# Performance work log

Hardware: AMD Instinct MI355X
Metric: run time of the kernel (lower is better)

Reference implementation:

```python
import jax, jax.numpy as jnp
import numpy as np

DIM = 96
D_STATE = 16
EXPAND = 2
D_INNER = EXPAND * DIM


def _scan_1d(x, delta, A, Bm, Cm, D):
    # x, delta: [b, l, d]; A: [d, n]; Bm, Cm: [b, l, n]; D: [d]
    delta = jax.nn.softplus(delta)
    dA = jnp.exp(jnp.einsum('bld,dn->bldn', delta, A))          # [b,l,d,n]
    dBx = jnp.einsum('bld,bln,bld->bldn', delta, Bm, x)         # delta*B*x

    def step(h, inp):
        dA_t, dBx_t, C_t = inp
        h = dA_t * h + dBx_t                                     # [b,d,n]
        y = jnp.einsum('bdn,bn->bd', h, C_t)
        return h, y

    b, l, d = x.shape
    n = A.shape[1]
    h0 = jnp.zeros((b, d, n), dtype=x.dtype)
    xs = (jnp.moveaxis(dA, 1, 0), jnp.moveaxis(dBx, 1, 0), jnp.moveaxis(Cm, 1, 0))
    _, ys = jax.lax.scan(step, h0, xs)                           # ys: [l,b,d]
    y = jnp.moveaxis(ys, 0, 1)                                   # [b,l,d]
    return y + x * D


def setup_inputs() -> dict:
    key = jax.random.key(0)
    ks = jax.random.split(key, 6)
    x = jax.random.normal(ks[0], (4, 64, 64, DIM), dtype=jnp.float32)
    d_out = D_INNER * 2 + D_STATE * 2 + D_INNER
    W_in = jax.random.normal(ks[1], (d_out, DIM), dtype=jnp.float32) * 0.02
    w_conv = jax.random.normal(ks[2], (D_INNER, 1, 3), dtype=jnp.float32) * 0.1
    W_fuse = jax.random.normal(ks[3], (D_INNER, D_INNER * 2, 1), dtype=jnp.float32) * 0.02
    W_out = jax.random.normal(ks[4], (DIM, D_INNER), dtype=jnp.float32) * 0.02
    A_log = jnp.log(jnp.tile(jnp.arange(1, D_STATE + 1, dtype=jnp.float32), (D_INNER, 1)))
    D = jnp.ones((D_INNER,), dtype=jnp.float32)
    return {"x": x, "W_in": W_in, "w_conv": w_conv, "W_fuse": W_fuse,
            "W_out": W_out, "A_log": A_log, "D": D}


def reference(x, W_in, w_conv, W_fuse, W_out, A_log, D):
    B, H, W, C = x.shape
    di, n = A_log.shape
    proj = x @ W_in.T
    x_inner, z, B_ssm, C_ssm, delta = jnp.split(
        proj, [di, 2 * di, 2 * di + n, 2 * di + 2 * n], axis=-1)
    # depthwise conv1d over length-1 sequences (kernel=3, pad=1): only center tap
    x_conv = jax.nn.silu(x_inner * w_conv[:, 0, 1])
    A = -jnp.exp(A_log)
    # horizontal scan: rows of length W
    y_h = _scan_1d(x_conv.reshape(B * H, W, di), delta.reshape(B * H, W, di), A,
                   B_ssm.reshape(B * H, W, n), C_ssm.reshape(B * H, W, n), D)
    y_h = y_h.reshape(B, H, W, di)
    # vertical scan: columns of length H
    xv = jnp.transpose(x_conv, (0, 2, 1, 3)).reshape(B * W, H, di)
    dv = jnp.transpose(delta, (0, 2, 1, 3)).reshape(B * W, H, di)
    Bv = jnp.transpose(B_ssm, (0, 2, 1, 3)).reshape(B * W, H, n)
    Cv = jnp.transpose(C_ssm, (0, 2, 1, 3)).reshape(B * W, H, n)
    y_v = _scan_1d(xv, dv, A, Bv, Cv, D).reshape(B, W, H, di)
    y_v = jnp.transpose(y_v, (0, 2, 1, 3))
    y_cat = jnp.concatenate([y_h, y_v], axis=-1)                 # [B,H,W,2*di]
    # 1x1 conv on length-1 sequences == linear map
    y_fused = jnp.einsum('bhwk,dk->bhwd', y_cat, W_fuse[:, :, 0])
    y_fused = y_fused * jax.nn.silu(z)
    return y_fused @ W_out.T
```

## Files before the change

kernel.cpp:

```cpp
#include <hip/hip_runtime.h>
#include <math.h>

#define NT    16384
#define CIN   96
#define DI    192
#define NS    16
#define SEQ   64
#define NSEQ  256

typedef __attribute__((ext_vector_type(8))) short bf16x8;
typedef __attribute__((ext_vector_type(4))) float f32x4;

__device__ __forceinline__ float silu_f(float v) {
    return v * (1.0f / (1.0f + __expf(-v)));
}

__device__ __forceinline__ float softplus_f(float v) {
    return fmaxf(v, 0.0f) + log1pf(__expf(-fabsf(v)));
}

__device__ __forceinline__ unsigned short bf16_rn(float f) {
    unsigned int u = __float_as_uint(f);
    u += 0x7FFFu + ((u >> 16) & 1u);
    return (unsigned short)(u >> 16);
}
__device__ __forceinline__ float bf16f(unsigned short h) {
    return __uint_as_float(((unsigned int)h) << 16);
}

__device__ __forceinline__ void split8(const float* __restrict__ src,
                                       bf16x8* dH, bf16x8* dL) {
    const float4 v0 = *reinterpret_cast<const float4*>(src);
    const float4 v1 = *reinterpret_cast<const float4*>(src + 4);
    const float f[8] = {v0.x, v0.y, v0.z, v0.w, v1.x, v1.y, v1.z, v1.w};
    unsigned short h8[8], l8[8];
    #pragma unroll
    for (int j = 0; j < 8; ++j) {
        h8[j] = bf16_rn(f[j]);
        l8[j] = bf16_rn(f[j] - bf16f(h8[j]));
    }
    *dH = *reinterpret_cast<bf16x8*>(h8);
    *dL = *reinterpret_cast<bf16x8*>(l8);
}

__global__ __launch_bounds__(256) void kw_split(
    const float* __restrict__ Wf, const float* __restrict__ Wout,
    unsigned short* __restrict__ WfH, unsigned short* __restrict__ WfL,
    unsigned short* __restrict__ WoH, unsigned short* __restrict__ WoL)
{
    const int i = blockIdx.x * 256 + threadIdx.x;
    if (i < 192 * 384) {
        const float v = Wf[i];
        const unsigned short h = bf16_rn(v);
        WfH[i] = h; WfL[i] = bf16_rn(v - bf16f(h));
    }
    if (i < 96 * 192) {
        const float v = Wout[i];
        const unsigned short h = bf16_rn(v);
        WoH[i] = h; WoL[i] = bf16_rn(v - bf16f(h));
    }
}

__global__ __launch_bounds__(256) void k1_proj(
    const float* __restrict__ x, const float* __restrict__ Win,
    const float* __restrict__ wconv,
    float* __restrict__ xc, float* __restrict__ sz,
    float* __restrict__ Bc, float* __restrict__ Cc, float* __restrict__ dt)
{
    __shared__ bf16x8 AsH[64 * 13], AsL[64 * 13];
    __shared__ bf16x8 BsH[32 * 13], BsL[32 * 13];

    const int tid = threadIdx.x;
    const int lane = tid & 63;
    const int w = tid >> 6;
    const int wm = w & 1;
    const int wn = w >> 1;
    const int r = lane & 15;
    const int g = lane >> 4;
    const int t0 = blockIdx.x * 64;
    const int n0 = blockIdx.y * 32;

    #pragma unroll
    for (int it = 0; it < 3; ++it) {
        const int slot = tid + it * 256;
        const int row = slot / 12, seg = slot - row * 12;
        split8(&x[(size_t)(t0 + row) * CIN + seg * 8], &AsH[row * 13 + seg], &AsL[row * 13 + seg]);
    }
    #pragma unroll
    for (int it = 0; it < 2; ++it) {
        const int slot = tid + it * 256;
        if (slot < 384) {
            const int row = slot / 12, seg = slot - row * 12;
            split8(&Win[(size_t)(n0 + row) * CIN + seg * 8], &BsH[row * 13 + seg], &BsL[row * 13 + seg]);
        }
    }
    __syncthreads();

    f32x4 acc[2];
    acc[0] = (f32x4){0.f, 0.f, 0.f, 0.f};
    acc[1] = (f32x4){0.f, 0.f, 0.f, 0.f};

    #pragma unroll
    for (int ks = 0; ks < 3; ++ks) {
        const int sg = ks * 4 + g;
        bf16x8 aH[2], aL[2];
        #pragma unroll
        for (int i = 0; i < 2; ++i) {
            const int row = wm * 32 + i * 16 + r;
            aH[i] = AsH[row * 13 + sg];
            aL[i] = AsL[row * 13 + sg];
        }
        const int brow = wn * 16 + r;
        const bf16x8 bH = BsH[brow * 13 + sg];
        const bf16x8 bL = BsL[brow * 13 + sg];
        #pragma unroll
        for (int i = 0; i < 2; ++i) {
            acc[i] = __builtin_amdgcn_mfma_f32_16x16x32_bf16(aH[i], bH, acc[i], 0, 0, 0);
            acc[i] = __builtin_amdgcn_mfma_f32_16x16x32_bf16(aH[i], bL, acc[i], 0, 0, 0);
            acc[i] = __builtin_amdgcn_mfma_f32_16x16x32_bf16(aL[i], bH, acc[i], 0, 0, 0);
        }
    }

    const int cb = n0 + wn * 16;
    const int c = cb + r;
    #pragma unroll
    for (int i = 0; i < 2; ++i) {
        const int tr0 = t0 + wm * 32 + i * 16 + g * 4;
        if (cb < DI) {
            const float wcv = wconv[c * 3 + 1];
            #pragma unroll
            for (int q = 0; q < 4; ++q)
                xc[(tr0 + q) * DI + c] = silu_f(acc[i][q] * wcv);
        } else if (cb < 2 * DI) {
            #pragma unroll
            for (int q = 0; q < 4; ++q)
                sz[(tr0 + q) * DI + c - DI] = silu_f(acc[i][q]);
        } else if (cb < 2 * DI + NS) {
            #pragma unroll
            for (int q = 0; q < 4; ++q)
                Bc[(tr0 + q) * NS + r] = acc[i][q];
        } else if (cb < 2 * DI + 2 * NS) {
            #pragma unroll
            for (int q = 0; q < 4; ++q)
                Cc[(tr0 + q) * NS + r] = acc[i][q];
        } else {
            #pragma unroll
            for (int q = 0; q < 4; ++q)
                dt[(tr0 + q) * DI + c - 2 * DI - 2 * NS] = softplus_f(acc[i][q]);
        }
    }
}

__global__ __launch_bounds__(192) void k2_scan(
    const float* __restrict__ xc, const float* __restrict__ dt,
    const float* __restrict__ Bc, const float* __restrict__ Cc,
    const float* __restrict__ Dvec,
    unsigned short* __restrict__ yhH, unsigned short* __restrict__ yhL,
    unsigned short* __restrict__ yvH, unsigned short* __restrict__ yvL)
{
    const int d = threadIdx.x;
    const int sid = blockIdx.x;
    const bool vert = sid >= NSEQ;
    const int s0 = vert ? (sid - NSEQ) : sid;

    float h[NS];
    #pragma unroll
    for (int n = 0; n < NS; ++n) h[n] = 0.f;
    const float dD = Dvec[d];
    unsigned short* __restrict__ youtH = vert ? yvH : yhH;
    unsigned short* __restrict__ youtL = vert ? yvL : yhL;

    const int base = vert ? (((s0 >> 6) << 12) + (s0 & 63)) : (s0 * 64);
    const int stride = vert ? 64 : 1;

    int t = base;
    float dtv = dt[t * DI + d];
    float xv  = xc[t * DI + d];
    float Bn[NS], Cn[NS];
    *reinterpret_cast<float4*>(&Bn[0])  = *reinterpret_cast<const float4*>(&Bc[t * NS + 0]);
    *reinterpret_cast<float4*>(&Bn[4])  = *reinterpret_cast<const float4*>(&Bc[t * NS + 4]);
    *reinterpret_cast<float4*>(&Bn[8])  = *reinterpret_cast<const float4*>(&Bc[t * NS + 8]);
    *reinterpret_cast<float4*>(&Bn[12]) = *reinterpret_cast<const float4*>(&Bc[t * NS + 12]);
    *reinterpret_cast<float4*>(&Cn[0])  = *reinterpret_cast<const float4*>(&Cc[t * NS + 0]);
    *reinterpret_cast<float4*>(&Cn[4])  = *reinterpret_cast<const float4*>(&Cc[t * NS + 4]);
    *reinterpret_cast<float4*>(&Cn[8])  = *reinterpret_cast<const float4*>(&Cc[t * NS + 8]);
    *reinterpret_cast<float4*>(&Cn[12]) = *reinterpret_cast<const float4*>(&Cc[t * NS + 12]);

    #pragma unroll 2
    for (int s = 0; s < SEQ; ++s) {
        const int tn = (s + 1 < SEQ) ? (t + stride) : t;
        const float dtv_n = dt[tn * DI + d];
        const float xv_n  = xc[tn * DI + d];
        float Bn2[NS], Cn2[NS];
        *reinterpret_cast<float4*>(&Bn2[0])  = *reinterpret_cast<const float4*>(&Bc[tn * NS + 0]);
        *reinterpret_cast<float4*>(&Bn2[4])  = *reinterpret_cast<const float4*>(&Bc[tn * NS + 4]);
        *reinterpret_cast<float4*>(&Bn2[8])  = *reinterpret_cast<const float4*>(&Bc[tn * NS + 8]);
        *reinterpret_cast<float4*>(&Bn2[12]) = *reinterpret_cast<const float4*>(&Bc[tn * NS + 12]);
        *reinterpret_cast<float4*>(&Cn2[0])  = *reinterpret_cast<const float4*>(&Cc[tn * NS + 0]);
        *reinterpret_cast<float4*>(&Cn2[4])  = *reinterpret_cast<const float4*>(&Cc[tn * NS + 4]);
        *reinterpret_cast<float4*>(&Cn2[8])  = *reinterpret_cast<const float4*>(&Cc[tn * NS + 8]);
        *reinterpret_cast<float4*>(&Cn2[12]) = *reinterpret_cast<const float4*>(&Cc[tn * NS + 12]);

        const float dtx = dtv * xv;
        const float r = __expf(-dtv);
        float p[NS];
        p[0] = r;           p[1] = r * r;
        p[2] = p[1] * p[0]; p[3] = p[1] * p[1];
        p[4] = p[3] * p[0]; p[5] = p[3] * p[1];
        p[6] = p[3] * p[2]; p[7] = p[3] * p[3];
        p[8]  = p[7] * p[0]; p[9]  = p[7] * p[1];
        p[10] = p[7] * p[2]; p[11] = p[7] * p[3];
        p[12] = p[7] * p[4]; p[13] = p[7] * p[5];
        p[14] = p[7] * p[6]; p[15] = p[7] * p[7];

        float yy[4] = {0.f, 0.f, 0.f, 0.f};
        #pragma unroll
        for (int n = 0; n < NS; ++n) {
            h[n] = fmaf(p[n], h[n], Bn[n] * dtx);
            yy[n & 3] = fmaf(h[n], Cn[n], yy[n & 3]);
        }
        const float y = (yy[0] + yy[1]) + (yy[2] + yy[3]);
        const float yval = fmaf(xv, dD, y);
        const unsigned short hi = bf16_rn(yval);
        youtH[t * DI + d] = hi;
        youtL[t * DI + d] = bf16_rn(yval - bf16f(hi));

        t = tn; dtv = dtv_n; xv = xv_n;
        #pragma unroll
        for (int n = 0; n < NS; ++n) { Bn[n] = Bn2[n]; Cn[n] = Cn2[n]; }
    }
}

#define FSP 200
__global__ __launch_bounds__(256) void k34_fused(
    const unsigned short* __restrict__ yhH, const unsigned short* __restrict__ yhL,
    const unsigned short* __restrict__ yvH, const unsigned short* __restrict__ yvL,
    const unsigned short* __restrict__ WfH, const unsigned short* __restrict__ WfL,
    const unsigned short* __restrict__ WoH, const unsigned short* __restrict__ WoL,
    const float* __restrict__ sz,
    float* __restrict__ out)
{
    __shared__ bf16x8 AsH[32 * 5], AsL[32 * 5];
    __shared__ bf16x8 BsH[192 * 5], BsL[192 * 5];
    __shared__ bf16x8 WsH[96 * 5], WsL[96 * 5];
    __shared__ unsigned short fsH[32 * FSP], fsL[32 * FSP];

    const int tid = threadIdx.x;
    const int lane = tid & 63;
    const int w = tid >> 6;
    const int wm = w & 1;
    const int wn = w >> 1;
    const int r = lane & 15;
    const int g = lane >> 4;
    const int t0 = blockIdx.x * 32;

    f32x4 acc[6];
    #pragma unroll
    for (int nt = 0; nt < 6; ++nt) acc[nt] = (f32x4){0.f, 0.f, 0.f, 0.f};

    for (int s = 0; s < 12; ++s) {
        const int ph = s >= 6;
        const int koff = (s - ph * 6) * 32;
        __syncthreads();
        {
            const int plane = tid >> 7;
            const int slot = tid & 127;
            const int row = slot >> 2, seg = slot & 3;
            const unsigned short* __restrict__ src =
                ph ? (plane ? yvL : yvH) : (plane ? yhL : yhH);
            bf16x8* dst = plane ? AsL : AsH;
            dst[row * 5 + seg] = *reinterpret_cast<const bf16x8*>(&src[(t0 + row) * DI + koff + seg * 8]);
        }
        #pragma unroll
        for (int it = 0; it < 6; ++it) {
            const int slot = tid + it * 256;
            const int plane = slot >= 768;
            const int s2 = plane ? slot - 768 : slot;
            const int row = s2 >> 2, seg = s2 & 3;
            const unsigned short* __restrict__ src = plane ? WfL : WfH;
            bf16x8* dst = plane ? BsL : BsH;
            dst[row * 5 + seg] = *reinterpret_cast<const bf16x8*>(&src[row * 384 + ph * 192 + koff + seg * 8]);
        }
        __syncthreads();
        const bf16x8 aH = AsH[(wm * 16 + r) * 5 + g];
        const bf16x8 aL = AsL[(wm * 16 + r) * 5 + g];
        #pragma unroll
        for (int nt = 0; nt < 6; ++nt) {
            const int brow = wn * 96 + nt * 16 + r;
            const bf16x8 bH = BsH[brow * 5 + g];
            const bf16x8 bL = BsL[brow * 5 + g];
            acc[nt] = __builtin_amdgcn_mfma_f32_16x16x32_bf16(aH, bH, acc[nt], 0, 0, 0);
            acc[nt] = __builtin_amdgcn_mfma_f32_16x16x32_bf16(aH, bL, acc[nt], 0, 0, 0);
            acc[nt] = __builtin_amdgcn_mfma_f32_16x16x32_bf16(aL, bH, acc[nt], 0, 0, 0);
        }
    }

    __syncthreads();
    #pragma unroll
    for (int nt = 0; nt < 6; ++nt) {
        const int c = wn * 96 + nt * 16 + r;
        #pragma unroll
        for (int q = 0; q < 4; ++q) {
            const int trow = wm * 16 + g * 4 + q;
            const float v = acc[nt][q] * sz[(t0 + trow) * DI + c];
            const unsigned short hi = bf16_rn(v);
            fsH[trow * FSP + c] = hi;
            fsL[trow * FSP + c] = bf16_rn(v - bf16f(hi));
        }
    }

    f32x4 oacc[3];
    #pragma unroll
    for (int nt = 0; nt < 3; ++nt) oacc[nt] = (f32x4){0.f, 0.f, 0.f, 0.f};

    for (int s = 0; s < 6; ++s) {
        const int koff = s * 32;
        __syncthreads();
        #pragma unroll
        for (int it = 0; it < 3; ++it) {
            const int slot = tid + it * 256;
            const int plane = slot >= 384;
            const int s2 = plane ? slot - 384 : slot;
            const int row = s2 >> 2, seg = s2 & 3;
            const unsigned short* __restrict__ src = plane ? WoL : WoH;
            bf16x8* dst = plane ? WsL : WsH;
            dst[row * 5 + seg] = *reinterpret_cast<const bf16x8*>(&src[row * 192 + koff + seg * 8]);
        }
        __syncthreads();
        const int arow = wm * 16 + r;
        const bf16x8 aH = *reinterpret_cast<const bf16x8*>(&fsH[arow * FSP + koff + g * 8]);
        const bf16x8 aL = *reinterpret_cast<const bf16x8*>(&fsL[arow * FSP + koff + g * 8]);
        #pragma unroll
        for (int nt = 0; nt < 3; ++nt) {
            const int brow = wn * 48 + nt * 16 + r;
            const bf16x8 bH = WsH[brow * 5 + g];
            const bf16x8 bL = WsL[brow * 5 + g];
            oacc[nt] = __builtin_amdgcn_mfma_f32_16x16x32_bf16(aH, bH, oacc[nt], 0, 0, 0);
            oacc[nt] = __builtin_amdgcn_mfma_f32_16x16x32_bf16(aH, bL, oacc[nt], 0, 0, 0);
            oacc[nt] = __builtin_amdgcn_mfma_f32_16x16x32_bf16(aL, bH, oacc[nt], 0, 0, 0);
        }
    }

    #pragma unroll
    for (int nt = 0; nt < 3; ++nt) {
        const int c = wn * 48 + nt * 16 + r;
        #pragma unroll
        for (int q = 0; q < 4; ++q) {
            out[(t0 + wm * 16 + g * 4 + q) * 96 + c] = oacc[nt][q];
        }
    }
}

extern "C" void kernel_launch(void* const* d_in, const int* in_sizes, int n_in,
                              void* d_out, int out_size, void* d_ws, size_t ws_size,
                              hipStream_t stream)
{
    const float* x     = (const float*)d_in[0];
    const float* Win   = (const float*)d_in[1];
    const float* wconv = (const float*)d_in[2];
    const float* Wf    = (const float*)d_in[3];
    const float* Wout  = (const float*)d_in[4];
    const float* Dvec  = (const float*)d_in[6];
    float* out = (float*)d_out;

    float* ws  = (float*)d_ws;
    float* xc  = ws;
    float* dt  = xc + (size_t)NT * DI;
    float* sz  = dt + (size_t)NT * DI;
    float* Bc  = sz + (size_t)NT * DI;
    float* Cc  = Bc + (size_t)NT * NS;
    unsigned short* yhH = (unsigned short*)(Cc + (size_t)NT * NS);
    unsigned short* yhL = yhH + (size_t)NT * DI;
    unsigned short* yvH = yhL + (size_t)NT * DI;
    unsigned short* yvL = yvH + (size_t)NT * DI;
    unsigned short* WfH = yvL + (size_t)NT * DI;
    unsigned short* WfL = WfH + (size_t)192 * 384;
    unsigned short* WoH = WfL + (size_t)192 * 384;
    unsigned short* WoL = WoH + (size_t)96 * 192;

    kw_split<<<288, 256, 0, stream>>>(Wf, Wout, WfH, WfL, WoH, WoL);
    k1_proj<<<dim3(NT / 64, 19), 256, 0, stream>>>(x, Win, wconv, xc, sz, Bc, Cc, dt);
    k2_scan<<<2 * NSEQ, 192, 0, stream>>>(xc, dt, Bc, Cc, Dvec, yhH, yhL, yvH, yvL);
    k34_fused<<<NT / 32, 256, 0, stream>>>(yhH, yhL, yvH, yvL, WfH, WfL, WoH, WoL, sz, out);
}
```

Before: 91.90 us.

## Pre-split x and W_in to bf16 hi/lo once and widen projection N-tile

Moves the fp32-to-bf16 hi/lo splitting of x and W_in out of the projection GEMM into a separate pre-pass kernel, so each projection block loads ready-made bf16 planes instead of re-splitting x for every N-tile. The projection N-tile doubles from 32 to 64 columns, halving the number of blocks that reload and convert the same x rows, with a bounds guard for the ragged last tile. The cost is an extra global round trip for the split x planes and more shared memory per block.

After: 93.86 us. 1.02x slower.

```diff
diff --git a/kernel.cpp b/kernel.cpp
--- a/kernel.cpp
+++ b/kernel.cpp
@@ -28,27 +28,33 @@
     return __uint_as_float(((unsigned int)h) << 16);
 }
 
-__device__ __forceinline__ void split8(const float* __restrict__ src,
-                                       bf16x8* dH, bf16x8* dL) {
-    const float4 v0 = *reinterpret_cast<const float4*>(src);
-    const float4 v1 = *reinterpret_cast<const float4*>(src + 4);
-    const float f[8] = {v0.x, v0.y, v0.z, v0.w, v1.x, v1.y, v1.z, v1.w};
-    unsigned short h8[8], l8[8];
-    #pragma unroll
-    for (int j = 0; j < 8; ++j) {
-        h8[j] = bf16_rn(f[j]);
-        l8[j] = bf16_rn(f[j] - bf16f(h8[j]));
-    }
-    *dH = *reinterpret_cast<bf16x8*>(h8);
-    *dL = *reinterpret_cast<bf16x8*>(l8);
-}
-
-__global__ __launch_bounds__(256) void kw_split(
+__global__ __launch_bounds__(256) void kx_split(
+    const float* __restrict__ x, const float* __restrict__ Win,
     const float* __restrict__ Wf, const float* __restrict__ Wout,
+    unsigned short* __restrict__ xH, unsigned short* __restrict__ xL,
+    unsigned short* __restrict__ WiH, unsigned short* __restrict__ WiL,
     unsigned short* __restrict__ WfH, unsigned short* __restrict__ WfL,
     unsigned short* __restrict__ WoH, unsigned short* __restrict__ WoL)
 {
     const int i = blockIdx.x * 256 + threadIdx.x;
+    const int i4 = i * 4;
+    {
+        const float4 v = *reinterpret_cast<const float4*>(&x[i4]);
+        unsigned short h[4], l[4];
+        const float vv[4] = {v.x, v.y, v.z, v.w};
+        #pragma unroll
+        for (int j = 0; j < 4; ++j) {
+            h[j] = bf16_rn(vv[j]);
+            l[j] = bf16_rn(vv[j] - bf16f(h[j]));
+        }
+        *reinterpret_cast<uint2*>(&xH[i4]) = *reinterpret_cast<uint2*>(h);
+        *reinterpret_cast<uint2*>(&xL[i4]) = *reinterpret_cast<uint2*>(l);
+    }
+    if (i < 608 * 96) {
+        const float v = Win[i];
+        const unsigned short h = bf16_rn(v);
+        WiH[i] = h; WiL[i] = bf16_rn(v - bf16f(h));
+    }
     if (i < 192 * 384) {
         const float v = Wf[i];
         const unsigned short h = bf16_rn(v);
@@ -62,13 +68,14 @@
 }
 
 __global__ __launch_bounds__(256) void k1_proj(
-    const float* __restrict__ x, const float* __restrict__ Win,
+    const unsigned short* __restrict__ xH, const unsigned short* __restrict__ xL,
+    const unsigned short* __restrict__ WiH, const unsigned short* __restrict__ WiL,
     const float* __restrict__ wconv,
     float* __restrict__ xc, float* __restrict__ sz,
     float* __restrict__ Bc, float* __restrict__ Cc, float* __restrict__ dt)
 {
     __shared__ bf16x8 AsH[64 * 13], AsL[64 * 13];
-    __shared__ bf16x8 BsH[32 * 13], BsL[32 * 13];
+    __shared__ bf16x8 BsH[64 * 13], BsL[64 * 13];
 
     const int tid = threadIdx.x;
     const int lane = tid & 63;
@@ -78,75 +85,94 @@
     const int r = lane & 15;
     const int g = lane >> 4;
     const int t0 = blockIdx.x * 64;
-    const int n0 = blockIdx.y * 32;
-
-    #pragma unroll
-    for (int it = 0; it < 3; ++it) {
+    const int n0 = blockIdx.y * 64;
+
+    #pragma unroll
+    for (int it = 0; it < 6; ++it) {
         const int slot = tid + it * 256;
-        const int row = slot / 12, seg = slot - row * 12;
-        split8(&x[(size_t)(t0 + row) * CIN + seg * 8], &AsH[row * 13 + seg], &AsL[row * 13 + seg]);
-    }
-    #pragma unroll
-    for (int it = 0; it < 2; ++it) {
+        const int plane = slot >= 768;
+        const int s2 = plane ? slot - 768 : slot;
+        const int row = s2 / 12, seg = s2 - row * 12;
+        const unsigned short* __restrict__ src = plane ? xL : xH;
+        bf16x8* dst = plane ? AsL : AsH;
+        dst[row * 13 + seg] = *reinterpret_cast<const bf16x8*>(&src[(size_t)(t0 + row) * CIN + seg * 8]);
+    }
+    #pragma unroll
+    for (int it = 0; it < 6; ++it) {
         const int slot = tid + it * 256;
-        if (slot < 384) {
-            const int row = slot / 12, seg = slot - row * 12;
-            split8(&Win[(size_t)(n0 + row) * CIN + seg * 8], &BsH[row * 13 + seg], &BsL[row * 13 + seg]);
+        const int plane = slot >= 768;
+        const int s2 = plane ? slot - 768 : slot;
+        const int row = s2 / 12, seg = s2 - row * 12;
+        if (n0 + row < 608) {
+            const unsigned short* __restrict__ src = plane ? WiL : WiH;
+            bf16x8* dst = plane ? BsL : BsH;
+            dst[row * 13 + seg] = *reinterpret_cast<const bf16x8*>(&src[(size_t)(n0 + row) * CIN + seg * 8]);
         }
     }
     __syncthreads();
 
-    f32x4 acc[2];
-    acc[0] = (f32x4){0.f, 0.f, 0.f, 0.f};
-    acc[1] = (f32x4){0.f, 0.f, 0.f, 0.f};
+    f32x4 acc[2][2];
+    #pragma unroll
+    for (int i = 0; i < 2; ++i)
+        #pragma unroll
+        for (int nt = 0; nt < 2; ++nt) acc[i][nt] = (f32x4){0.f, 0.f, 0.f, 0.f};
 
     #pragma unroll
     for (int ks = 0; ks < 3; ++ks) {
         const int sg = ks * 4 + g;
-        bf16x8 aH[2], aL[2];
+        bf16x8 aH[2], aL[2], bH[2], bL[2];
         #pragma unroll
         for (int i = 0; i < 2; ++i) {
             const int row = wm * 32 + i * 16 + r;
             aH[i] = AsH[row * 13 + sg];
             aL[i] = AsL[row * 13 + sg];
         }
-        const int brow = wn * 16 + r;
-        const bf16x8 bH = BsH[brow * 13 + sg];
-        const bf16x8 bL = BsL[brow * 13 + sg];
+        #pragma unroll
+        for (int nt = 0; nt < 2; ++nt) {
+            const int row = wn * 32 + nt * 16 + r;
+            bH[nt] = BsH[row * 13 + sg];
+            bL[nt] = BsL[row * 13 + sg];
+        }
+        #pragma unroll
+        for (int nt = 0; nt < 2; ++nt)
+            #pragma unroll
+            for (int i = 0; i < 2; ++i) {
+                acc[i][nt] = __builtin_amdgcn_mfma_f32_16x16x32_bf16(aH[i], bH[nt], acc[i][nt], 0, 0, 0);
+                acc[i][nt] = __builtin_amdgcn_mfma_f32_16x16x32_bf16(aH[i], bL[nt], acc[i][nt], 0, 0, 0);
+                acc[i][nt] = __builtin_amdgcn_mfma_f32_16x16x32_bf16(aL[i], bH[nt], acc[i][nt], 0, 0, 0);
+            }
+    }
+
+    #pragma unroll
+    for (int nt = 0; nt < 2; ++nt) {
+        const int cb = n0 + wn * 32 + nt * 16;
+        if (cb >= 608) continue;
+        const int c = cb + r;
         #pragma unroll
         for (int i = 0; i < 2; ++i) {
-            acc[i] = __builtin_amdgcn_mfma_f32_16x16x32_bf16(aH[i], bH, acc[i], 0, 0, 0);
-            acc[i] = __builtin_amdgcn_mfma_f32_16x16x32_bf16(aH[i], bL, acc[i], 0, 0, 0);
-            acc[i] = __builtin_amdgcn_mfma_f32_16x16x32_bf16(aL[i], bH, acc[i], 0, 0, 0);
-        }
-    }
-
-    const int cb = n0 + wn * 16;
-    const int c = cb + r;
-    #pragma unroll
-    for (int i = 0; i < 2; ++i) {
-        const int tr0 = t0 + wm * 32 + i * 16 + g * 4;
-        if (cb < DI) {
-            const float wcv = wconv[c * 3 + 1];
-            #pragma unroll
-            for (int q = 0; q < 4; ++q)
-                xc[(tr0 + q) * DI + c] = silu_f(acc[i][q] * wcv);
-        } else if (cb < 2 * DI) {
-            #pragma unroll
-            for (int q = 0; q < 4; ++q)
-                sz[(tr0 + q) * DI + c - DI] = silu_f(acc[i][q]);
-        } else if (cb < 2 * DI + NS) {
-            #pragma unroll
-            for (int q = 0; q < 4; ++q)
-                Bc[(tr0 + q) * NS + r] = acc[i][q];
-        } else if (cb < 2 * DI + 2 * NS) {
-            #pragma unroll
-            for (int q = 0; q < 4; ++q)
-                Cc[(tr0 + q) * NS + r] = acc[i][q];
-        } else {
-            #pragma unroll
-            for (int q = 0; q < 4; ++q)
-                dt[(tr0 + q) * DI + c - 2 * DI - 2 * NS] = softplus_f(acc[i][q]);
+            const int tr0 = t0 + wm * 32 + i * 16 + g * 4;
+            if (cb < DI) {
+                const float wcv = wconv[c * 3 + 1];
+                #pragma unroll
+                for (int q = 0; q < 4; ++q)
+                    xc[(tr0 + q) * DI + c] = silu_f(acc[i][nt][q] * wcv);
+            } else if (cb < 2 * DI) {
+                #pragma unroll
+                for (int q = 0; q < 4; ++q)
+                    sz[(tr0 + q) * DI + c - DI] = silu_f(acc[i][nt][q]);
+            } else if (cb < 2 * DI + NS) {
+                #pragma unroll
+                for (int q = 0; q < 4; ++q)
+                    Bc[(tr0 + q) * NS + r] = acc[i][nt][q];
+            } else if (cb < 2 * DI + 2 * NS) {
+                #pragma unroll
+                for (int q = 0; q < 4; ++q)
+                    Cc[(tr0 + q) * NS + r] = acc[i][nt][q];
+            } else {
+                #pragma unroll
+                for (int q = 0; q < 4; ++q)
+                    dt[(tr0 + q) * DI + c - 2 * DI - 2 * NS] = softplus_f(acc[i][nt][q]);
+            }
         }
     }
 }
@@ -377,9 +403,14 @@
     unsigned short* WfL = WfH + (size_t)192 * 384;
     unsigned short* WoH = WfL + (size_t)192 * 384;
     unsigned short* WoL = WoH + (size_t)96 * 192;
-
-    kw_split<<<288, 256, 0, stream>>>(Wf, Wout, WfH, WfL, WoH, WoL);
-    k1_proj<<<dim3(NT / 64, 19), 256, 0, stream>>>(x, Win, wconv, xc, sz, Bc, Cc, dt);
+    unsigned short* WiH = WoL + (size_t)96 * 192;
+    unsigned short* WiL = WiH + (size_t)608 * 96;
+    unsigned short* xH  = WiL + (size_t)608 * 96;
+    unsigned short* xL  = xH  + (size_t)NT * CIN;
+
+    kx_split<<<(NT * CIN) / 1024, 256, 0, stream>>>(x, Win, Wf, Wout,
+                                                    xH, xL, WiH, WiL, WfH, WfL, WoH, WoL);
+    k1_proj<<<dim3(NT / 64, 10), 256, 0, stream>>>(xH, xL, WiH, WiL, wconv, xc, sz, Bc, Cc, dt);
     k2_scan<<<2 * NSEQ, 192, 0, stream>>>(xc, dt, Bc, Cc, Dvec, yhH, yhL, yvH, yvL);
     k34_fused<<<NT / 32, 256, 0, stream>>>(yhH, yhL, yvH, yvL, WfH, WfL, WoH, WoL, sz, out);
 }
```

## Recompute z-gate projection inside fused output kernel instead of storing silu(z)

Applied to the files above, without the earlier changes.

Moves the z-branch of the input projection out of k1_proj and into k34_fused, which now computes x·Wz with split-bf16 MFMAs and applies silu in registers instead of reading an NT×192 fp32 sz buffer. A new kx_split kernel pre-splits x into bf16 hi/lo planes, and kw_split also splits the Wz slice of W_in. This removes the write and read of sz and shrinks the k1_proj grid. In exchange it adds an extra kernel launch, writes and reads the x hi/lo planes, and adds MFMA work and shared-memory staging to k34_fused.

Measured after the change: 94.45 us. 2.8% more time.

```diff
diff --git a/kernel.cpp b/kernel.cpp
--- a/kernel.cpp
+++ b/kernel.cpp
@@ -43,10 +43,29 @@
     *dL = *reinterpret_cast<bf16x8*>(l8);
 }
 
+__global__ __launch_bounds__(256) void kx_split(
+    const float* __restrict__ x,
+    unsigned short* __restrict__ xH, unsigned short* __restrict__ xL)
+{
+    const int i4 = (blockIdx.x * 256 + threadIdx.x) * 4;
+    const float4 v = *reinterpret_cast<const float4*>(&x[i4]);
+    unsigned short h[4], l[4];
+    const float vv[4] = {v.x, v.y, v.z, v.w};
+    #pragma unroll
+    for (int j = 0; j < 4; ++j) {
+        h[j] = bf16_rn(vv[j]);
+        l[j] = bf16_rn(vv[j] - bf16f(h[j]));
+    }
+    *reinterpret_cast<uint2*>(&xH[i4]) = *reinterpret_cast<uint2*>(h);
+    *reinterpret_cast<uint2*>(&xL[i4]) = *reinterpret_cast<uint2*>(l);
+}
+
 __global__ __launch_bounds__(256) void kw_split(
     const float* __restrict__ Wf, const float* __restrict__ Wout,
+    const float* __restrict__ Win,
     unsigned short* __restrict__ WfH, unsigned short* __restrict__ WfL,
-    unsigned short* __restrict__ WoH, unsigned short* __restrict__ WoL)
+    unsigned short* __restrict__ WoH, unsigned short* __restrict__ WoL,
+    unsigned short* __restrict__ WzH, unsigned short* __restrict__ WzL)
 {
     const int i = blockIdx.x * 256 + threadIdx.x;
     if (i < 192 * 384) {
@@ -59,12 +78,17 @@
         const unsigned short h = bf16_rn(v);
         WoH[i] = h; WoL[i] = bf16_rn(v - bf16f(h));
     }
+    if (i < 192 * 96) {
+        const float v = Win[192 * 96 + i];
+        const unsigned short h = bf16_rn(v);
+        WzH[i] = h; WzL[i] = bf16_rn(v - bf16f(h));
+    }
 }
 
 __global__ __launch_bounds__(256) void k1_proj(
     const float* __restrict__ x, const float* __restrict__ Win,
     const float* __restrict__ wconv,
-    float* __restrict__ xc, float* __restrict__ sz,
+    float* __restrict__ xc,
     float* __restrict__ Bc, float* __restrict__ Cc, float* __restrict__ dt)
 {
     __shared__ bf16x8 AsH[64 * 13], AsL[64 * 13];
@@ -78,7 +102,8 @@
     const int r = lane & 15;
     const int g = lane >> 4;
     const int t0 = blockIdx.x * 64;
-    const int n0 = blockIdx.y * 32;
+    const int ty = (blockIdx.y < 6) ? blockIdx.y : blockIdx.y + 6;
+    const int n0 = ty * 32;
 
     #pragma unroll
     for (int it = 0; it < 3; ++it) {
@@ -131,10 +156,6 @@
             #pragma unroll
             for (int q = 0; q < 4; ++q)
                 xc[(tr0 + q) * DI + c] = silu_f(acc[i][q] * wcv);
-        } else if (cb < 2 * DI) {
-            #pragma unroll
-            for (int q = 0; q < 4; ++q)
-                sz[(tr0 + q) * DI + c - DI] = silu_f(acc[i][q]);
         } else if (cb < 2 * DI + NS) {
             #pragma unroll
             for (int q = 0; q < 4; ++q)
@@ -235,9 +256,10 @@
 __global__ __launch_bounds__(256) void k34_fused(
     const unsigned short* __restrict__ yhH, const unsigned short* __restrict__ yhL,
     const unsigned short* __restrict__ yvH, const unsigned short* __restrict__ yvL,
+    const unsigned short* __restrict__ xH, const unsigned short* __restrict__ xL,
+    const unsigned short* __restrict__ WzH, const unsigned short* __restrict__ WzL,
     const unsigned short* __restrict__ WfH, const unsigned short* __restrict__ WfL,
     const unsigned short* __restrict__ WoH, const unsigned short* __restrict__ WoL,
-    const float* __restrict__ sz,
     float* __restrict__ out)
 {
     __shared__ bf16x8 AsH[32 * 5], AsL[32 * 5];
@@ -254,6 +276,45 @@
     const int g = lane >> 4;
     const int t0 = blockIdx.x * 32;
 
+    f32x4 zacc[6];
+    #pragma unroll
+    for (int nt = 0; nt < 6; ++nt) zacc[nt] = (f32x4){0.f, 0.f, 0.f, 0.f};
+
+    for (int s = 0; s < 3; ++s) {
+        const int koff = s * 32;
+        __syncthreads();
+        {
+            const int plane = tid >> 7;
+            const int slot = tid & 127;
+            const int row = slot >> 2, seg = slot & 3;
+            const unsigned short* __restrict__ src = plane ? xL : xH;
+            bf16x8* dst = plane ? AsL : AsH;
+            dst[row * 5 + seg] = *reinterpret_cast<const bf16x8*>(&src[(size_t)(t0 + row) * CIN + koff + seg * 8]);
+        }
+        #pragma unroll
+        for (int it = 0; it < 6; ++it) {
+            const int slot = tid + it * 256;
+            const int plane = slot >= 768;
+            const int s2 = plane ? slot - 768 : slot;
+            const int row = s2 >> 2, seg = s2 & 3;
+            const unsigned short* __restrict__ src = plane ? WzL : WzH;
+            bf16x8* dst = plane ? BsL : BsH;
+            dst[row * 5 + seg] = *reinterpret_cast<const bf16x8*>(&src[row * CIN + koff + seg * 8]);
+        }
+        __syncthreads();
+        const bf16x8 aH = AsH[(wm * 16 + r) * 5 + g];
+        const bf16x8 aL = AsL[(wm * 16 + r) * 5 + g];
+        #pragma unroll
+        for (int nt = 0; nt < 6; ++nt) {
+            const int brow = wn * 96 + nt * 16 + r;
+            const bf16x8 bH = BsH[brow * 5 + g];
+            const bf16x8 bL = BsL[brow * 5 + g];
+            zacc[nt] = __builtin_amdgcn_mfma_f32_16x16x32_bf16(aH, bH, zacc[nt], 0, 0, 0);
+            zacc[nt] = __builtin_amdgcn_mfma_f32_16x16x32_bf16(aH, bL, zacc[nt], 0, 0, 0);
+            zacc[nt] = __builtin_amdgcn_mfma_f32_16x16x32_bf16(aL, bH, zacc[nt], 0, 0, 0);
+        }
+    }
+
     f32x4 acc[6];
     #pragma unroll
     for (int nt = 0; nt < 6; ++nt) acc[nt] = (f32x4){0.f, 0.f, 0.f, 0.f};
@@ -302,7 +363,7 @@
         #pragma unroll
         for (int q = 0; q < 4; ++q) {
             const int trow = wm * 16 + g * 4 + q;
-            const float v = acc[nt][q] * sz[(t0 + trow) * DI + c];
+            const float v = acc[nt][q] * silu_f(zacc[nt][q]);
             const unsigned short hi = bf16_rn(v);
             fsH[trow * FSP + c] = hi;
             fsL[trow * FSP + c] = bf16_rn(v - bf16f(hi));
@@ -366,8 +427,7 @@
     float* ws  = (float*)d_ws;
     float* xc  = ws;
     float* dt  = xc + (size_t)NT * DI;
-    float* sz  = dt + (size_t)NT * DI;
-    float* Bc  = sz + (size_t)NT * DI;
+    float* Bc  = dt + (size_t)NT * DI;
     float* Cc  = Bc + (size_t)NT * NS;
     unsigned short* yhH = (unsigned short*)(Cc + (size_t)NT * NS);
     unsigned short* yhL = yhH + (size_t)NT * DI;
@@ -377,9 +437,15 @@
     unsigned short* WfL = WfH + (size_t)192 * 384;
     unsigned short* WoH = WfL + (size_t)192 * 384;
     unsigned short* WoL = WoH + (size_t)96 * 192;
-
-    kw_split<<<288, 256, 0, stream>>>(Wf, Wout, WfH, WfL, WoH, WoL);
-    k1_proj<<<dim3(NT / 64, 19), 256, 0, stream>>>(x, Win, wconv, xc, sz, Bc, Cc, dt);
+    unsigned short* WzH = WoL + (size_t)96 * 192;
+    unsigned short* WzL = WzH + (size_t)192 * 96;
+    unsigned short* xH  = WzL + (size_t)192 * 96;
+    unsigned short* xL  = xH  + (size_t)NT * CIN;
+
+    kx_split<<<(NT * CIN) / 1024, 256, 0, stream>>>(x, xH, xL);
+    kw_split<<<288, 256, 0, stream>>>(Wf, Wout, Win, WfH, WfL, WoH, WoL, WzH, WzL);
+    k1_proj<<<dim3(NT / 64, 13), 256, 0, stream>>>(x, Win, wconv, xc, Bc, Cc, dt);
     k2_scan<<<2 * NSEQ, 192, 0, stream>>>(xc, dt, Bc, Cc, Dvec, yhH, yhL, yvH, yvL);
-    k34_fused<<<NT / 32, 256, 0, stream>>>(yhH, yhL, yvH, yvL, WfH, WfL, WoH, WoL, sz, out);
-}
+    k34_fused<<<NT / 32, 256, 0, stream>>>(yhH, yhL, yvH, yvL, xH, xL, WzH, WzL,
+                                           WfH, WfL, WoH, WoL, out);
+}
```
